# Optimization experiments

Hardware: AMD Instinct MI355X
Metric: run time of the kernel (lower is better)

Reference implementation:

```python
import jax, jax.numpy as jnp
import numpy as np

L, B, D, H = 2048, 2, 1024, 16
HD = D // H
DFF = 4 * D
EPS = 1e-5


def layernorm(x, g, b):
    mu = jnp.mean(x, axis=-1, keepdims=True)
    var = jnp.mean((x - mu) ** 2, axis=-1, keepdims=True)
    return (x - mu) * jax.lax.rsqrt(var + EPS) * g + b


def setup_inputs() -> dict:
    key = jax.random.key(0)
    ks = jax.random.split(key, 12)
    s = 0.02
    return {
        "x": jax.random.normal(ks[0], (L, B, D), jnp.float32),
        "ln1_g": jnp.ones((D,), jnp.float32),
        "ln1_b": jnp.zeros((D,), jnp.float32),
        "w_attn": jax.random.normal(ks[1], (D, 3 * D), jnp.float32) * s,
        "b_attn": jnp.zeros((3 * D,), jnp.float32),
        "w_proj": jax.random.normal(ks[2], (D, D), jnp.float32) * s,
        "b_proj": jnp.zeros((D,), jnp.float32),
        "ln2_g": jnp.ones((D,), jnp.float32),
        "ln2_b": jnp.zeros((D,), jnp.float32),
        "w_fc": jax.random.normal(ks[3], (D, DFF), jnp.float32) * s,
        "b_fc": jnp.zeros((DFF,), jnp.float32),
        "w_out": jax.random.normal(ks[4], (DFF, D), jnp.float32) * s,
        "b_out": jnp.zeros((D,), jnp.float32),
    }


def reference(x, ln1_g, ln1_b, w_attn, b_attn, w_proj, b_proj,
              ln2_g, ln2_b, w_fc, b_fc, w_out, b_out):
    # x: [L, B, D]
    h = layernorm(x, ln1_g, ln1_b)
    qkv = h @ w_attn + b_attn                     # [L, B, 3D]
    qkv = jnp.transpose(qkv, (1, 0, 2))            # [B, L, 3D]
    q, k, v = jnp.split(qkv, 3, axis=-1)

    def split_heads(t):                            # [B, L, D] -> [B, H, L, hd]
        return jnp.transpose(t.reshape(B, L, H, HD), (0, 2, 1, 3))

    q, k, v = split_heads(q), split_heads(k), split_heads(v)
    # present: stack of (key, value), key in [B,H,L,hd] layout (post transpose-back)
    present = jnp.stack((k, v))                    # [2, B, H, L, hd]

    scores = jnp.einsum('bhqd,bhkd->bhqk', q, k) / jnp.sqrt(jnp.float32(HD))
    w = jax.nn.softmax(scores, axis=-1)
    a = jnp.einsum('bhqk,bhkd->bhqd', w, v)        # [B, H, L, hd]
    a = jnp.transpose(a, (0, 2, 1, 3)).reshape(B, L, D)
    a = a @ w_proj + b_proj                        # [B, L, D]
    a = jnp.transpose(a, (1, 0, 2))                # [L, B, D]

    x = x + a
    m = jax.nn.gelu(layernorm(x, ln2_g, ln2_b) @ w_fc + b_fc) @ w_out + b_out
    x = x + m
    return x, present
```

## Files before the change

### kernel.cpp

```cpp
#include <hip/hip_runtime.h>
#include <stdint.h>

#define L_SEQ 2048
#define BATCH 2
#define DIM   1024
#define NH    16
#define HDIM  64
#define DFF_  4096
#define ROWS  (L_SEQ*BATCH)

#define QSCALE 0.18033688011112042f

typedef __attribute__((ext_vector_type(8))) short  bf16x8;
typedef __attribute__((ext_vector_type(4))) float  floatx4;

__device__ __forceinline__ unsigned short f2bf(float f) {
    union { float f; uint32_t u; } x; x.f = f;
    uint32_t r = x.u + 0x7fffu + ((x.u >> 16) & 1u);
    return (unsigned short)(r >> 16);
}
__device__ __forceinline__ float bf2f(unsigned short b) {
    union { uint32_t u; float f; } x; x.u = ((uint32_t)b) << 16;
    return x.f;
}
__device__ __forceinline__ uint32_t fbits(float f) {
    union { float f; uint32_t u; } x; x.f = f; return x.u;
}

__device__ __forceinline__ void load_lds16(const unsigned short* g, unsigned short* l) {
    __builtin_amdgcn_global_load_lds(
        (const __attribute__((address_space(1))) unsigned int*)g,
        (__attribute__((address_space(3))) unsigned int*)l, 16, 0, 0);
}

__global__ __launch_bounds__(256)
void transpose_all(const float* __restrict__ s0, unsigned short* __restrict__ d0,
                   const float* __restrict__ s1, unsigned short* __restrict__ d1,
                   const float* __restrict__ s2, unsigned short* __restrict__ d2,
                   const float* __restrict__ s3, unsigned short* __restrict__ d3)
{
    const int id = blockIdx.x;
    const float* src; unsigned short* dst; int K, N, local;
    if (id < 3072)      { src = s0; dst = d0; K = 1024; N = 3072; local = id; }
    else if (id < 4096) { src = s1; dst = d1; K = 1024; N = 1024; local = id - 3072; }
    else if (id < 8192) { src = s2; dst = d2; K = 1024; N = 4096; local = id - 4096; }
    else                { src = s3; dst = d3; K = 4096; N = 1024; local = id - 8192; }
    const int nN = N >> 5;
    const int bk = (local / nN) * 32, bn = (local % nN) * 32;

    __shared__ float tile[32][36];
    const int t = threadIdx.x;
    const int r = t >> 3, c4 = (t & 7) * 4;
    *(float4*)&tile[r][c4] = *(const float4*)(src + (size_t)(bk + r) * N + bn + c4);
    __syncthreads();
    ushort4 o;
    o.x = f2bf(tile[c4 + 0][r]);
    o.y = f2bf(tile[c4 + 1][r]);
    o.z = f2bf(tile[c4 + 2][r]);
    o.w = f2bf(tile[c4 + 3][r]);
    *(ushort4*)(dst + (size_t)(bn + r) * K + bk + c4) = o;
}

template<int INBF16>
__global__ __launch_bounds__(256)
void ln_rows(const void* __restrict__ xin, const float* __restrict__ g,
             const float* __restrict__ bta, unsigned short* __restrict__ out)
{
    const int row = blockIdx.x;
    const int t = threadIdx.x;
    float4 v;
    if (INBF16) {
        const ushort4 u = ((const ushort4*)((const unsigned short*)xin + (size_t)row * DIM))[t];
        v.x = bf2f(u.x); v.y = bf2f(u.y); v.z = bf2f(u.z); v.w = bf2f(u.w);
    } else {
        v = ((const float4*)((const float*)xin + (size_t)row * DIM))[t];
    }
    float s  = v.x + v.y + v.z + v.w;
    float s2 = v.x*v.x + v.y*v.y + v.z*v.z + v.w*v.w;
#pragma unroll
    for (int d = 1; d < 64; d <<= 1) { s += __shfl_xor(s, d, 64); s2 += __shfl_xor(s2, d, 64); }
    __shared__ float ss[4], ss2[4];
    const int w = t >> 6, lane = t & 63;
    if (lane == 0) { ss[w] = s; ss2[w] = s2; }
    __syncthreads();
    s  = ss[0] + ss[1] + ss[2] + ss[3];
    s2 = ss2[0] + ss2[1] + ss2[2] + ss2[3];
    const float mu   = s * (1.0f / DIM);
    const float var  = s2 * (1.0f / DIM) - mu * mu;
    const float rstd = rsqrtf(var + 1e-5f);
    const float4 gv = ((const float4*)g)[t];
    const float4 bv = ((const float4*)bta)[t];
    ushort4 o;
    o.x = f2bf((v.x - mu) * rstd * gv.x + bv.x);
    o.y = f2bf((v.y - mu) * rstd * gv.y + bv.y);
    o.z = f2bf((v.z - mu) * rstd * gv.z + bv.z);
    o.w = f2bf((v.w - mu) * rstd * gv.w + bv.w);
    *(ushort4*)(out + (size_t)row * DIM + t * 4) = o;
}

template<int GELU, int RESID, int OUTBF16, int MI, int SPLITK>
__global__ __launch_bounds__(256)
void gemm_bt(const unsigned short* __restrict__ A,
             const unsigned short* __restrict__ Bt,
             const float* __restrict__ bias,
             const void* __restrict__ resid,
             void* __restrict__ outp,
             float* __restrict__ part,
             int M, int N, int K)
{
    __shared__ unsigned short As[MI * 32 * 32];
    __shared__ unsigned short Bs[128 * 32];
    const int t = threadIdx.x;
    const int w = t >> 6, lane = t & 63;
    const int quad = lane >> 4, l16 = lane & 15;
    const int wm = (w >> 1) * (MI * 16), wn = (w & 1) * 64;
    const int bm = blockIdx.x * (MI * 32), bn = blockIdx.y * 128;

    const int srow = lane >> 2;
    const int scol = (lane & 3) * 8;

    const unsigned short* Ab = A  + (size_t)bm * K;
    const unsigned short* Bb = Bt + (size_t)bn * K;

    floatx4 acc[MI][4] = {};

    const int kspan = (SPLITK > 1) ? (K / SPLITK) : K;
    const int k0    = (SPLITK > 1) ? blockIdx.z * kspan : 0;

    for (int kc = k0; kc < k0 + kspan; kc += 32) {
        __syncthreads();
#pragma unroll
        for (int i = 0; i < MI / 2; ++i) {
            const int r0 = (i * 4 + w) * 16;
            load_lds16(Ab + (size_t)(r0 + srow) * K + kc + scol, As + r0 * 32);
        }
#pragma unroll
        for (int i = 0; i < 2; ++i) {
            const int r0 = (i * 4 + w) * 16;
            load_lds16(Bb + (size_t)(r0 + srow) * K + kc + scol, Bs + r0 * 32);
        }
        __syncthreads();
        bf16x8 af[MI], bf[4];
#pragma unroll
        for (int i = 0; i < MI; ++i) af[i] = *(const bf16x8*)(As + (wm + i*16 + l16) * 32 + quad * 8);
#pragma unroll
        for (int j = 0; j < 4; ++j) bf[j] = *(const bf16x8*)(Bs + (wn + j*16 + l16) * 32 + quad * 8);
#pragma unroll
        for (int i = 0; i < MI; ++i)
#pragma unroll
            for (int j = 0; j < 4; ++j)
                acc[i][j] = __builtin_amdgcn_mfma_f32_16x16x32_bf16(af[i], bf[j], acc[i][j], 0, 0, 0);
    }

    if (SPLITK > 1 && blockIdx.z > 0) {
        float* po = part + (size_t)(blockIdx.z - 1) * ((size_t)M * N);
#pragma unroll
        for (int i = 0; i < MI; ++i)
#pragma unroll
            for (int j = 0; j < 4; ++j) {
                const int col = bn + wn + j*16 + l16;
#pragma unroll
                for (int r = 0; r < 4; ++r) {
                    const int row = bm + wm + i*16 + quad*4 + r;
                    po[(size_t)row * N + col] = acc[i][j][r];
                }
            }
        return;
    }

#pragma unroll
    for (int i = 0; i < MI; ++i) {
#pragma unroll
        for (int j = 0; j < 4; ++j) {
            const int col = bn + wn + j*16 + l16;
            const float bv = bias[col];
#pragma unroll
            for (int r = 0; r < 4; ++r) {
                const int row = bm + wm + i*16 + quad*4 + r;
                float v = acc[i][j][r] + bv;
                if (RESID == 1) v += ((const float*)resid)[(size_t)row * N + col];
                if (RESID == 2) v += bf2f(((const unsigned short*)resid)[(size_t)row * N + col]);
                if (GELU) {
                    const float u = v;
                    float c = 2.302204225929898f * (u + 0.044715f * u * u * u);
                    c = fminf(c, 80.f);
                    const float e = exp2f(c);
                    v = u * (e / (1.0f + e));
                }
                if (OUTBF16) ((unsigned short*)outp)[(size_t)row * N + col] = f2bf(v);
                else         ((float*)outp)[(size_t)row * N + col] = v;
            }
        }
    }
}

#define SWZ32(p) ((p) ^ ((((p) >> 7) & 3) << 4))

template<int GELU, int RESID, int OUTBF16, int SPLITK>
__global__ __launch_bounds__(512, 2)
void gemm256b(const unsigned short* __restrict__ A,
              const unsigned short* __restrict__ Bt,
              const float* __restrict__ bias,
              const void* __restrict__ resid,
              void* __restrict__ outp,
              float* __restrict__ part,
              int M, int N, int K, int nbx)
{
    __shared__ unsigned short lds[32768];
    const int t = threadIdx.x;
    const int w = t >> 6, lane = t & 63;
    const int quad = lane >> 4, l16 = lane & 15;
    const int wr = w >> 2, wc = w & 3;

    const int nwg = gridDim.x;
    const int cpx = nwg >> 3;
    const int bid = (blockIdx.x & 7) * cpx + (blockIdx.x >> 3);
    const int bm = (bid % nbx) * 256, bn = (bid / nbx) * 256;

    const unsigned short* Ab = A  + (size_t)bm * K;
    const unsigned short* Bb = Bt + (size_t)bn * K;

    const int sh   = SWZ32(t * 16);
    const int rp0  = sh >> 6;
    const int colE = (sh & 63) >> 1;
    const int w0 = rp0 & 63, hb = rp0 >> 6;
    const size_t bOff0 = (size_t)rp0 * K + colE;
    const size_t bOff1 = (size_t)(128 + rp0) * K + colE;
    const size_t aOff0 = (size_t)(w0 + hb * 128)      * K + colE;
    const size_t aOff1 = (size_t)(w0 + hb * 128 + 64) * K + colE;

#define STGH(dstE_, srcp_, kta_, off_) \
    load_lds16((srcp_) + (size_t)(kta_) * 32 + (off_), lds + (dstE_) + w * 512)
#define BARF    do { __builtin_amdgcn_s_barrier(); asm volatile("" ::: "memory"); } while (0)
#define CL_PRE  do { asm volatile("s_waitcnt lgkmcnt(0)" ::: "memory");    \
                     __builtin_amdgcn_sched_barrier(0);                    \
                     __builtin_amdgcn_s_setprio(1); } while (0)
#define CL_POST do { __builtin_amdgcn_s_setprio(0);                        \
                     __builtin_amdgcn_sched_barrier(0); } while (0)

    floatx4 acc[8][4] = {};
    const int nt  = ((SPLITK > 1) ? (K / SPLITK) : K) >> 5;
    const int ktb = (SPLITK > 1) ? blockIdx.y * nt : 0;

    STGH(0,     Ab, ktb,     aOff0);  STGH(4096,  Ab, ktb,     aOff1);
    STGH(8192,  Bb, ktb,     bOff0);  STGH(12288, Bb, ktb,     bOff1);
    STGH(16384, Ab, ktb + 1, aOff0);  STGH(20480, Ab, ktb + 1, aOff1);
    STGH(24576, Bb, ktb + 1, bOff0);  STGH(28672, Bb, ktb + 1, bOff1);
    asm volatile("s_waitcnt vmcnt(4)" ::: "memory");
    BARF;

    for (int i = 0; i < nt; ++i) {
        const int cb = i & 1;
        const int i1 = (i + 1 < nt) ? i + 1 : nt - 1;
        const int i2 = (i + 2 < nt) ? i + 2 : nt - 1;
        const int oA = cb * 16384, oB = oA + 8192;
        const int xA = (cb ^ 1) * 16384;
        const char* Abase = (const char*)lds + cb * 32768;
        const char* Bbase = Abase + 16384;
        bf16x8 af[4], bf[4];

        STGH(xA + 4096, Ab, ktb + i1, aOff1);
#pragma unroll
        for (int mi = 0; mi < 4; ++mi) {
            const int p = (wr * 64 + mi * 16 + l16) * 64 + quad * 16;
            af[mi] = *(const bf16x8*)(Abase + SWZ32(p));
        }
#pragma unroll
        for (int nj = 0; nj < 4; ++nj) {
            const int p = (wc * 64 + nj * 16 + l16) * 64 + quad * 16;
            bf[nj] = *(const bf16x8*)(Bbase + SWZ32(p));
        }
        BARF;
        CL_PRE;
#pragma unroll
        for (int mi = 0; mi < 4; ++mi)
#pragma unroll
            for (int nj = 0; nj < 4; ++nj)
                acc[mi][nj] = __builtin_amdgcn_mfma_f32_16x16x32_bf16(af[mi], bf[nj], acc[mi][nj], 0, 0, 0);
        CL_POST;
        BARF;

        STGH(oB,        Bb, ktb + i2, bOff0);
        STGH(oB + 4096, Bb, ktb + i2, bOff1);
        STGH(oA,        Ab, ktb + i2, aOff0);
#pragma unroll
        for (int mi = 0; mi < 4; ++mi) {
            const int p = (128 + wr * 64 + mi * 16 + l16) * 64 + quad * 16;
            af[mi] = *(const bf16x8*)(Abase + SWZ32(p));
        }
        BARF;
        CL_PRE;
#pragma unroll
        for (int mi = 0; mi < 4; ++mi)
#pragma unroll
            for (int nj = 0; nj < 4; ++nj)
                acc[4 + mi][nj] = __builtin_amdgcn_mfma_f32_16x16x32_bf16(af[mi], bf[nj], acc[4 + mi][nj], 0, 0, 0);
        CL_POST;
        asm volatile("s_waitcnt vmcnt(3)" ::: "memory");
        BARF;
    }

    if (SPLITK > 1 && blockIdx.y > 0) {
        float* po = part + (size_t)(blockIdx.y - 1) * ((size_t)M * N);
#pragma unroll
        for (int mi = 0; mi < 8; ++mi)
#pragma unroll
            for (int nj = 0; nj < 4; ++nj) {
                const int col = bn + wc * 64 + nj * 16 + l16;
#pragma unroll
                for (int r = 0; r < 4; ++r) {
                    const int row = bm + wr * 128 + mi * 16 + quad * 4 + r;
                    po[(size_t)row * N + col] = acc[mi][nj][r];
                }
            }
        return;
    }

#pragma unroll
    for (int mi = 0; mi < 8; ++mi) {
#pragma unroll
        for (int nj = 0; nj < 4; ++nj) {
            const int col = bn + wc * 64 + nj * 16 + l16;
            const float bv = bias[col];
#pragma unroll
            for (int r = 0; r < 4; ++r) {
                const int row = bm + wr * 128 + mi * 16 + quad * 4 + r;
                float v = acc[mi][nj][r] + bv;
                if (RESID == 1) v += ((const float*)resid)[(size_t)row * N + col];
                if (RESID == 2) v += bf2f(((const unsigned short*)resid)[(size_t)row * N + col]);
                if (GELU) {
                    const float u = v;
                    float c = 2.302204225929898f * (u + 0.044715f * u * u * u);
                    c = fminf(c, 80.f);
                    const float e = exp2f(c);
                    v = u * (e / (1.0f + e));
                }
                if (OUTBF16) ((unsigned short*)outp)[(size_t)row * N + col] = f2bf(v);
                else         ((float*)outp)[(size_t)row * N + col] = v;
            }
        }
    }
#undef STGH
#undef BARF
#undef CL_PRE
#undef CL_POST
}

__global__ __launch_bounds__(256)
void splitk_add(const float* __restrict__ part, float* __restrict__ outp)
{
    const size_t i = ((size_t)blockIdx.x * 256 + threadIdx.x) * 4;
    float4 a = *(const float4*)(outp + i);
    const float4 p = *(const float4*)(part + i);
    a.x += p.x; a.y += p.y; a.z += p.z; a.w += p.w;
    *(float4*)(outp + i) = a;
}

__global__ __launch_bounds__(256)
void split_qkv(const unsigned short* __restrict__ qkv,
               unsigned short* __restrict__ q, unsigned short* __restrict__ k,
               float* __restrict__ present)
{
    const size_t idx = (size_t)blockIdx.x * 256 + threadIdx.x;
    const int g8  = idx & 7;
    const int l   = (idx >> 3) & 2047;
    const int bh  = (idx >> 14) & 31;
    const int sel = (int)(idx >> 19);
    const int b = bh >> 4, h = bh & 15;
    const unsigned short* src = qkv + (size_t)(l * BATCH + b) * (3 * DIM) + sel * DIM + h * HDIM + g8 * 8;
    const uint4 val = *(const uint4*)src;
    const unsigned short* sv = (const unsigned short*)&val;
    if (sel == 0) {
        unsigned short ov[8];
#pragma unroll
        for (int j = 0; j < 8; ++j) ov[j] = f2bf(bf2f(sv[j]) * QSCALE);
        *(uint4*)(q + ((size_t)bh * L_SEQ + l) * HDIM + g8 * 8) = *(uint4*)ov;
    } else {
        *(uint4*)(k + ((size_t)bh * L_SEQ + l) * HDIM + g8 * 8) = val;
        float* p = present + (((size_t)b * NH + h) * L_SEQ + l) * HDIM + (size_t)g8 * 8;
        float4 f0, f1;
        f0.x = bf2f(sv[0]); f0.y = bf2f(sv[1]); f0.z = bf2f(sv[2]); f0.w = bf2f(sv[3]);
        f1.x = bf2f(sv[4]); f1.y = bf2f(sv[5]); f1.z = bf2f(sv[6]); f1.w = bf2f(sv[7]);
        ((float4*)p)[0] = f0; ((float4*)p)[1] = f1;
    }
}

__global__ __launch_bounds__(256)
void transpose_v(const unsigned short* __restrict__ qkv, unsigned short* __restrict__ vt,
                 float* __restrict__ present)
{
    __shared__ unsigned short tile[64][72];
    const int lt = blockIdx.x;
    const int bh = blockIdx.y;
    const int b = bh >> 4, h = bh & 15;
    const int t = threadIdx.x;
#pragma unroll
    for (int i = 0; i < 2; ++i) {
        const int idx = i * 256 + t;
        const int l = idx >> 3, c = (idx & 7) * 8;
        const uint4 val =
            *(const uint4*)(qkv + (size_t)((lt * 64 + l) * BATCH + b) * (3 * DIM) + 2 * DIM + h * HDIM + c);
        *(uint4*)(&tile[l][c]) = val;
        const unsigned short* sv = (const unsigned short*)&val;
        float* p = present + ((((size_t)BATCH + b) * NH + h) * L_SEQ + lt * 64 + l) * HDIM + c;
        float4 f0, f1;
        f0.x = bf2f(sv[0]); f0.y = bf2f(sv[1]); f0.z = bf2f(sv[2]); f0.w = bf2f(sv[3]);
        f1.x = bf2f(sv[4]); f1.y = bf2f(sv[5]); f1.z = bf2f(sv[6]); f1.w = bf2f(sv[7]);
        ((float4*)p)[0] = f0; ((float4*)p)[1] = f1;
    }
    __syncthreads();
#pragma unroll
    for (int i = 0; i < 2; ++i) {
        const int idx = i * 256 + t;
        const int d = idx >> 3, l0 = (idx & 7) * 8;
        const int kk = l0 >> 3;
        ushort4 o[2];
        unsigned short* ov = (unsigned short*)o;
#pragma unroll
        for (int jj = 0; jj < 8; ++jj) {
            const int j = (jj + kk) & 7;
            ov[j] = tile[l0 + j][d];
        }
        *(uint4*)(vt + ((size_t)bh * HDIM + d) * L_SEQ + lt * 64 + l0) = *(uint4*)o;
    }
}

__global__ __launch_bounds__(256, 4)
void attn_kernel(const unsigned short* __restrict__ Q,
                 const unsigned short* __restrict__ Kk,
                 const unsigned short* __restrict__ Vt,
                 unsigned short* __restrict__ Opart,
                 float* __restrict__ Lpart)
{
    const int qt = blockIdx.x;
    const int ks = blockIdx.y;
    const int bh = blockIdx.z;
    const int b = bh >> 4, h = bh & 15;
    const int t = threadIdx.x, w = t >> 6, lane = t & 63;
    const int quad = lane >> 4, l16 = lane & 15;

    __shared__ unsigned short Ks[64][72];
    __shared__ unsigned short Vts[64][72];
    __shared__ unsigned short Ps[4][32][72];

    const size_t head_off = (size_t)bh * L_SEQ * HDIM;
    const int q_base = qt * 128 + w * 32;
    const int kt0 = ks * 1024;

    bf16x8 qf[2][2];
#pragma unroll
    for (int nf = 0; nf < 2; ++nf)
#pragma unroll
        for (int ds = 0; ds < 2; ++ds)
            qf[nf][ds] = *(const bf16x8*)(Q + head_off + (size_t)(q_base + nf*16 + l16) * HDIM + ds*32 + quad*8);

    const int sr = t >> 3;
    const int sc = (t & 7) * 8;

    floatx4 o[4][2] = {};
    float l_i[2] = {0.f, 0.f};

    for (int kt = kt0; kt < kt0 + 1024; kt += 64) {
        __syncthreads();
#pragma unroll
        for (int i = 0; i < 2; ++i) {
            const int row = sr + i * 32;
            *(uint4*)(&Ks[row][sc])  = *(const uint4*)(Kk + head_off + (size_t)(kt + row) * HDIM + sc);
            *(uint4*)(&Vts[row][sc]) = *(const uint4*)(Vt + head_off + (size_t)row * L_SEQ + kt + sc);
        }
        __syncthreads();

        floatx4 s[4][2] = {};
#pragma unroll
        for (int ds = 0; ds < 2; ++ds)
#pragma unroll
            for (int jt = 0; jt < 4; ++jt) {
                const bf16x8 kf = *(const bf16x8*)(&Ks[jt*16 + l16][ds*32 + quad*8]);
                s[jt][0] = __builtin_amdgcn_mfma_f32_16x16x32_bf16(kf, qf[0][ds], s[jt][0], 0, 0, 0);
                s[jt][1] = __builtin_amdgcn_mfma_f32_16x16x32_bf16(kf, qf[1][ds], s[jt][1], 0, 0, 0);
            }

#pragma unroll
        for (int nf = 0; nf < 2; ++nf)
#pragma unroll
            for (int jt = 0; jt < 4; ++jt) {
                const float p0 = exp2f(s[jt][nf][0]);
                const float p1 = exp2f(s[jt][nf][1]);
                const float p2 = exp2f(s[jt][nf][2]);
                const float p3 = exp2f(s[jt][nf][3]);
                l_i[nf] += (p0 + p1) + (p2 + p3);
                uint2 pk;
                pk.x = __builtin_amdgcn_perm(fbits(p1), fbits(p0), 0x07060302u);
                pk.y = __builtin_amdgcn_perm(fbits(p3), fbits(p2), 0x07060302u);
                *(uint2*)(&Ps[w][nf*16 + l16][jt*16 + quad*4]) = pk;
            }

#pragma unroll
        for (int kk = 0; kk < 2; ++kk) {
            const bf16x8 pf0 = *(const bf16x8*)(&Ps[w][l16]     [kk*32 + quad*8]);
            const bf16x8 pf1 = *(const bf16x8*)(&Ps[w][16 + l16][kk*32 + quad*8]);
#pragma unroll
            for (int dt = 0; dt < 4; ++dt) {
                const bf16x8 vf = *(const bf16x8*)(&Vts[dt*16 + l16][kk*32 + quad*8]);
                o[dt][0] = __builtin_amdgcn_mfma_f32_16x16x32_bf16(vf, pf0, o[dt][0], 0, 0, 0);
                o[dt][1] = __builtin_amdgcn_mfma_f32_16x16x32_bf16(vf, pf1, o[dt][1], 0, 0, 0);
            }
        }
    }

    unsigned short* Op = Opart + (size_t)ks * ROWS * DIM;
#pragma unroll
    for (int nf = 0; nf < 2; ++nf) {
        float l = l_i[nf];
        l += __shfl_xor(l, 16, 64);
        l += __shfl_xor(l, 32, 64);
        const int q = q_base + nf*16 + l16;
        if (quad == 0)
            Lpart[((size_t)ks * 32 + bh) * L_SEQ + q] = l;
#pragma unroll
        for (int dt = 0; dt < 4; ++dt) {
            ushort4 ov;
            ov.x = f2bf(o[dt][nf][0]); ov.y = f2bf(o[dt][nf][1]);
            ov.z = f2bf(o[dt][nf][2]); ov.w = f2bf(o[dt][nf][3]);
            *(ushort4*)(Op + (size_t)(q * BATCH + b) * DIM + h * HDIM + dt*16 + quad*4) = ov;
        }
    }
}

__global__ __launch_bounds__(256)
void attn_merge(const unsigned short* __restrict__ Opart,
                const float* __restrict__ Lpart,
                unsigned short* __restrict__ Aout)
{
    const int row = blockIdx.x;
    const int q = row >> 1, b = row & 1;
    const int t = threadIdx.x;
    const int col = t * 4;
    const int h = col >> 6;
    const int bh = b * 16 + h;
    const float l0 = Lpart[(size_t)bh * L_SEQ + q];
    const float l1 = Lpart[((size_t)32 + bh) * L_SEQ + q];
    const float inv = 1.0f / (l0 + l1);
    const ushort4 o0 = *(const ushort4*)(Opart + (size_t)row * DIM + col);
    const ushort4 o1 = *(const ushort4*)(Opart + (size_t)ROWS * DIM + (size_t)row * DIM + col);
    ushort4 ov;
    ov.x = f2bf((bf2f(o0.x) + bf2f(o1.x)) * inv);
    ov.y = f2bf((bf2f(o0.y) + bf2f(o1.y)) * inv);
    ov.z = f2bf((bf2f(o0.z) + bf2f(o1.z)) * inv);
    ov.w = f2bf((bf2f(o0.w) + bf2f(o1.w)) * inv);
    *(ushort4*)(Aout + (size_t)row * DIM + col) = ov;
}

extern "C" void kernel_launch(void* const* d_in, const int* in_sizes, int n_in,
                              void* d_out, int out_size, void* d_ws, size_t ws_size,
                              hipStream_t stream)
{
    const float* x      = (const float*)d_in[0];
    const float* ln1_g  = (const float*)d_in[1];
    const float* ln1_b  = (const float*)d_in[2];
    const float* w_attn = (const float*)d_in[3];
    const float* b_attn = (const float*)d_in[4];
    const float* w_proj = (const float*)d_in[5];
    const float* b_proj = (const float*)d_in[6];
    const float* ln2_g  = (const float*)d_in[7];
    const float* ln2_b  = (const float*)d_in[8];
    const float* w_fc   = (const float*)d_in[9];
    const float* b_fc   = (const float*)d_in[10];
    const float* w_out  = (const float*)d_in[11];
    const float* b_out  = (const float*)d_in[12];

    char* ws = (char*)d_ws;
    unsigned short* watT   = (unsigned short*)(ws + 0);
    unsigned short* wprojT = (unsigned short*)(ws + 6291456);
    unsigned short* wfcT   = (unsigned short*)(ws + 8388608);
    unsigned short* woutT  = (unsigned short*)(ws + 16777216);
    unsigned short* h      = (unsigned short*)(ws + 25165824);
    unsigned short* qkv    = (unsigned short*)(ws + 33554432);
    unsigned short* opart  = (unsigned short*)(ws + 33554432);
    float*          lpart  = (float*)(ws + 50331648);
    unsigned short* mws    = (unsigned short*)(ws + 33554432);
    unsigned short* qw     = (unsigned short*)(ws + 58720256);
    unsigned short* kw     = (unsigned short*)(ws + 67108864);
    unsigned short* vt     = (unsigned short*)(ws + 75497472);
    unsigned short* aw     = (unsigned short*)(ws + 83886080);
    unsigned short* x2     = (unsigned short*)(ws + 92274688);
    float*          kpart  = (float*)(ws + 75497472);

    float* xout    = (float*)d_out;
    float* present = (float*)d_out + 4194304;

    transpose_all<<<12288, 256, 0, stream>>>(w_attn, watT, w_proj, wprojT, w_fc, wfcT, w_out, woutT);

    ln_rows<0><<<ROWS, 256, 0, stream>>>(x, ln1_g, ln1_b, h);
    gemm256b<0,0,1,1><<<dim3(192), 512, 0, stream>>>(h, watT, b_attn, nullptr, qkv, nullptr, ROWS, 3*DIM, DIM, 16);
    split_qkv<<<4096, 256, 0, stream>>>(qkv, qw, kw, present);
    transpose_v<<<dim3(32, 32), 256, 0, stream>>>(qkv, vt, present);
    attn_kernel<<<dim3(16, 2, 32), 256, 0, stream>>>(qw, kw, vt, opart, lpart);
    attn_merge<<<ROWS, 256, 0, stream>>>(opart, lpart, aw);
    gemm_bt<0,1,1,2,1><<<dim3(64, 8), 256, 0, stream>>>(aw, wprojT, b_proj, x, x2, nullptr, ROWS, DIM, DIM);
    ln_rows<1><<<ROWS, 256, 0, stream>>>(x2, ln2_g, ln2_b, h);
    gemm256b<1,0,1,1><<<dim3(256), 512, 0, stream>>>(h, wfcT, b_fc, nullptr, mws, nullptr, ROWS, DFF_, DIM, 16);
    gemm_bt<0,2,0,4,2><<<dim3(32, 8, 2), 256, 0, stream>>>(mws, woutT, b_out, x2, xout, kpart, ROWS, DIM, DFF_);
    splitk_add<<<4096, 256, 0, stream>>>(kpart, xout);
}
```

Before: 403.0 us.

## Double-buffer attention K/V tiles with async global-to-LDS loads and XOR swizzle

The attention kernel now stages K and V tiles into two LDS buffers using direct global-to-LDS loads (load_lds16), prefetching two tiles ahead so memory latency overlaps the MFMA work. The padded LDS arrays are replaced by an XOR-swizzled layout to avoid bank conflicts without padding. K fragments are loaded into registers before the buffer is refilled. This adds barriers per iteration and register pressure, and relies on vmcnt accounting being correct.

```diff
diff --git a/kernel.cpp b/kernel.cpp
--- a/kernel.cpp
+++ b/kernel.cpp
@@ -425,6 +425,8 @@
     }
 }
 
+#define SWZA(p) ((p) ^ ((((p) >> 7) & 7) << 4))
+
 __global__ __launch_bounds__(256, 4)
 void attn_kernel(const unsigned short* __restrict__ Q,
                  const unsigned short* __restrict__ Kk,
@@ -439,8 +441,8 @@
     const int t = threadIdx.x, w = t >> 6, lane = t & 63;
     const int quad = lane >> 4, l16 = lane & 15;
 
-    __shared__ unsigned short Ks[64][72];
-    __shared__ unsigned short Vts[64][72];
+    __shared__ unsigned short Ksb[2][4096];
+    __shared__ unsigned short Vsb[2][4096];
     __shared__ unsigned short Ps[4][32][72];
 
     const size_t head_off = (size_t)bh * L_SEQ * HDIM;
@@ -454,30 +456,58 @@
         for (int ds = 0; ds < 2; ++ds)
             qf[nf][ds] = *(const bf16x8*)(Q + head_off + (size_t)(q_base + nf*16 + l16) * HDIM + ds*32 + quad*8);
 
-    const int sr = t >> 3;
-    const int sc = (t & 7) * 8;
+    const int pA = t * 16, pB = 4096 + t * 16;
+    const int cA = (pA & 127) ^ (((pA >> 7) & 7) << 4);
+    const int cB = (pB & 127) ^ (((pB >> 7) & 7) << 4);
+    const int rA = pA >> 7, rB = pB >> 7;
+    const size_t kOff0 = (size_t)rA * HDIM + (cA >> 1);
+    const size_t kOff1 = (size_t)rB * HDIM + (cB >> 1);
+    const size_t vOff0 = (size_t)rA * L_SEQ + (cA >> 1);
+    const size_t vOff1 = (size_t)rB * L_SEQ + (cB >> 1);
+
+#define STAGE_K(buf_, kt_) do {                                            \
+        const unsigned short* g_ = Kk + head_off + (size_t)(kt_) * HDIM;   \
+        load_lds16(g_ + kOff0, Ksb[buf_] + w * 512);                       \
+        load_lds16(g_ + kOff1, Ksb[buf_] + 2048 + w * 512);                \
+    } while (0)
+#define STAGE_V(buf_, kt_) do {                                            \
+        const unsigned short* g_ = Vt + head_off + (kt_);                  \
+        load_lds16(g_ + vOff0, Vsb[buf_] + w * 512);                       \
+        load_lds16(g_ + vOff1, Vsb[buf_] + 2048 + w * 512);                \
+    } while (0)
 
     floatx4 o[4][2] = {};
     float l_i[2] = {0.f, 0.f};
 
-    for (int kt = kt0; kt < kt0 + 1024; kt += 64) {
+    STAGE_K(0, kt0);      STAGE_V(0, kt0);
+    STAGE_K(1, kt0 + 64); STAGE_V(1, kt0 + 64);
+    asm volatile("s_waitcnt vmcnt(4)" ::: "memory");
+    __syncthreads();
+
+    for (int it = 0; it < 16; ++it) {
+        const int cb = it & 1;
+        const int i2 = (it + 2 < 16) ? it + 2 : 15;
+        const unsigned short* Kl = Ksb[cb];
+        const unsigned short* Vl = Vsb[cb];
+
+        bf16x8 kf[2][4];
+#pragma unroll
+        for (int ds = 0; ds < 2; ++ds)
+#pragma unroll
+            for (int jt = 0; jt < 4; ++jt) {
+                const int p = (jt*16 + l16) * 128 + ds*64 + quad*16;
+                kf[ds][jt] = *(const bf16x8*)((const char*)Kl + SWZA(p));
+            }
         __syncthreads();
-#pragma unroll
-        for (int i = 0; i < 2; ++i) {
-            const int row = sr + i * 32;
-            *(uint4*)(&Ks[row][sc])  = *(const uint4*)(Kk + head_off + (size_t)(kt + row) * HDIM + sc);
-            *(uint4*)(&Vts[row][sc]) = *(const uint4*)(Vt + head_off + (size_t)row * L_SEQ + kt + sc);
-        }
-        __syncthreads();
+        STAGE_K(cb, kt0 + i2 * 64);
 
         floatx4 s[4][2] = {};
 #pragma unroll
         for (int ds = 0; ds < 2; ++ds)
 #pragma unroll
             for (int jt = 0; jt < 4; ++jt) {
-                const bf16x8 kf = *(const bf16x8*)(&Ks[jt*16 + l16][ds*32 + quad*8]);
-                s[jt][0] = __builtin_amdgcn_mfma_f32_16x16x32_bf16(kf, qf[0][ds], s[jt][0], 0, 0, 0);
-                s[jt][1] = __builtin_amdgcn_mfma_f32_16x16x32_bf16(kf, qf[1][ds], s[jt][1], 0, 0, 0);
+                s[jt][0] = __builtin_amdgcn_mfma_f32_16x16x32_bf16(kf[ds][jt], qf[0][ds], s[jt][0], 0, 0, 0);
+                s[jt][1] = __builtin_amdgcn_mfma_f32_16x16x32_bf16(kf[ds][jt], qf[1][ds], s[jt][1], 0, 0, 0);
             }
 
 #pragma unroll
@@ -501,11 +531,16 @@
             const bf16x8 pf1 = *(const bf16x8*)(&Ps[w][16 + l16][kk*32 + quad*8]);
 #pragma unroll
             for (int dt = 0; dt < 4; ++dt) {
-                const bf16x8 vf = *(const bf16x8*)(&Vts[dt*16 + l16][kk*32 + quad*8]);
+                const int p = (dt*16 + l16) * 128 + kk*64 + quad*16;
+                const bf16x8 vf = *(const bf16x8*)((const char*)Vl + SWZA(p));
                 o[dt][0] = __builtin_amdgcn_mfma_f32_16x16x32_bf16(vf, pf0, o[dt][0], 0, 0, 0);
                 o[dt][1] = __builtin_amdgcn_mfma_f32_16x16x32_bf16(vf, pf1, o[dt][1], 0, 0, 0);
             }
         }
+        __syncthreads();
+        STAGE_V(cb, kt0 + i2 * 64);
+        asm volatile("s_waitcnt vmcnt(4)" ::: "memory");
+        __syncthreads();
     }
 
     unsigned short* Op = Opart + (size_t)ks * ROWS * DIM;
@@ -525,6 +560,8 @@
             *(ushort4*)(Op + (size_t)(q * BATCH + b) * DIM + h * HDIM + dt*16 + quad*4) = ov;
         }
     }
+#undef STAGE_K
+#undef STAGE_V
 }
 
 __global__ __launch_bounds__(256)
```

After: 413.4 us. 1.03x slower.

## Prefetch K/V tiles into registers and XOR-swizzle attention LDS tiles

Applied to the files above, without the earlier changes.

The attention kernel now loads the next 64-key K and V^T tile into registers while computing on the current tile, then writes it to LDS after the compute. This hides global-load latency behind the MFMA work. The padded LDS arrays are replaced by unpadded 128-byte rows with an XOR swizzle for K, V^T and P, to avoid bank conflicts without the padding. The gemm256b template also loses its unused split-K and residual parameters, which is cleanup only. The prefetch adds registers and an extra barrier per iteration, which may lower occupancy.

```diff
diff --git a/kernel.cpp b/kernel.cpp
--- a/kernel.cpp
+++ b/kernel.cpp
@@ -196,14 +196,12 @@
 
 #define SWZ32(p) ((p) ^ ((((p) >> 7) & 3) << 4))
 
-template<int GELU, int RESID, int OUTBF16, int SPLITK>
+template<int GELU, int OUTBF16>
 __global__ __launch_bounds__(512, 2)
 void gemm256b(const unsigned short* __restrict__ A,
               const unsigned short* __restrict__ Bt,
               const float* __restrict__ bias,
-              const void* __restrict__ resid,
               void* __restrict__ outp,
-              float* __restrict__ part,
               int M, int N, int K, int nbx)
 {
     __shared__ unsigned short lds[32768];
@@ -239,13 +237,12 @@
                      __builtin_amdgcn_sched_barrier(0); } while (0)
 
     floatx4 acc[8][4] = {};
-    const int nt  = ((SPLITK > 1) ? (K / SPLITK) : K) >> 5;
-    const int ktb = (SPLITK > 1) ? blockIdx.y * nt : 0;
-
-    STGH(0,     Ab, ktb,     aOff0);  STGH(4096,  Ab, ktb,     aOff1);
-    STGH(8192,  Bb, ktb,     bOff0);  STGH(12288, Bb, ktb,     bOff1);
-    STGH(16384, Ab, ktb + 1, aOff0);  STGH(20480, Ab, ktb + 1, aOff1);
-    STGH(24576, Bb, ktb + 1, bOff0);  STGH(28672, Bb, ktb + 1, bOff1);
+    const int nt = K >> 5;
+
+    STGH(0,     Ab, 0, aOff0);  STGH(4096,  Ab, 0, aOff1);
+    STGH(8192,  Bb, 0, bOff0);  STGH(12288, Bb, 0, bOff1);
+    STGH(16384, Ab, 1, aOff0);  STGH(20480, Ab, 1, aOff1);
+    STGH(24576, Bb, 1, bOff0);  STGH(28672, Bb, 1, bOff1);
     asm volatile("s_waitcnt vmcnt(4)" ::: "memory");
     BARF;
 
@@ -259,7 +256,7 @@
         const char* Bbase = Abase + 16384;
         bf16x8 af[4], bf[4];
 
-        STGH(xA + 4096, Ab, ktb + i1, aOff1);
+        STGH(xA + 4096, Ab, i1, aOff1);
 #pragma unroll
         for (int mi = 0; mi < 4; ++mi) {
             const int p = (wr * 64 + mi * 16 + l16) * 64 + quad * 16;
@@ -280,9 +277,9 @@
         CL_POST;
         BARF;
 
-        STGH(oB,        Bb, ktb + i2, bOff0);
-        STGH(oB + 4096, Bb, ktb + i2, bOff1);
-        STGH(oA,        Ab, ktb + i2, aOff0);
+        STGH(oB,        Bb, i2, bOff0);
+        STGH(oB + 4096, Bb, i2, bOff1);
+        STGH(oA,        Ab, i2, aOff0);
 #pragma unroll
         for (int mi = 0; mi < 4; ++mi) {
             const int p = (128 + wr * 64 + mi * 16 + l16) * 64 + quad * 16;
@@ -300,22 +297,6 @@
         BARF;
     }
 
-    if (SPLITK > 1 && blockIdx.y > 0) {
-        float* po = part + (size_t)(blockIdx.y - 1) * ((size_t)M * N);
-#pragma unroll
-        for (int mi = 0; mi < 8; ++mi)
-#pragma unroll
-            for (int nj = 0; nj < 4; ++nj) {
-                const int col = bn + wc * 64 + nj * 16 + l16;
-#pragma unroll
-                for (int r = 0; r < 4; ++r) {
-                    const int row = bm + wr * 128 + mi * 16 + quad * 4 + r;
-                    po[(size_t)row * N + col] = acc[mi][nj][r];
-                }
-            }
-        return;
-    }
-
 #pragma unroll
     for (int mi = 0; mi < 8; ++mi) {
 #pragma unroll
@@ -326,8 +307,6 @@
             for (int r = 0; r < 4; ++r) {
                 const int row = bm + wr * 128 + mi * 16 + quad * 4 + r;
                 float v = acc[mi][nj][r] + bv;
-                if (RESID == 1) v += ((const float*)resid)[(size_t)row * N + col];
-                if (RESID == 2) v += bf2f(((const unsigned short*)resid)[(size_t)row * N + col]);
                 if (GELU) {
                     const float u = v;
                     float c = 2.302204225929898f * (u + 0.044715f * u * u * u);
@@ -425,6 +404,8 @@
     }
 }
 
+#define SWZA(p) ((p) ^ ((((p) >> 7) & 7) << 4))
+
 __global__ __launch_bounds__(256, 4)
 void attn_kernel(const unsigned short* __restrict__ Q,
                  const unsigned short* __restrict__ Kk,
@@ -439,9 +420,9 @@
     const int t = threadIdx.x, w = t >> 6, lane = t & 63;
     const int quad = lane >> 4, l16 = lane & 15;
 
-    __shared__ unsigned short Ks[64][72];
-    __shared__ unsigned short Vts[64][72];
-    __shared__ unsigned short Ps[4][32][72];
+    __shared__ unsigned short Ks[4096];
+    __shared__ unsigned short Vts[4096];
+    __shared__ unsigned short Ps[4][2048];
 
     const size_t head_off = (size_t)bh * L_SEQ * HDIM;
     const int q_base = qt * 128 + w * 32;
@@ -455,27 +436,43 @@
             qf[nf][ds] = *(const bf16x8*)(Q + head_off + (size_t)(q_base + nf*16 + l16) * HDIM + ds*32 + quad*8);
 
     const int sr = t >> 3;
-    const int sc = (t & 7) * 8;
+    const int c8 = t & 7;
+    const int sc = c8 * 8;
+    const int wb = sr * 128 + ((c8 * 16) ^ ((sr & 7) << 4));
+    const int wb2 = wb + 32 * 128;
+
+    uint4 kreg0, kreg1, vreg0, vreg1;
+
+#define LOAD_TILE(kt_) do {                                                              \
+        kreg0 = *(const uint4*)(Kk + head_off + (size_t)((kt_) + sr) * HDIM + sc);       \
+        kreg1 = *(const uint4*)(Kk + head_off + (size_t)((kt_) + sr + 32) * HDIM + sc);  \
+        vreg0 = *(const uint4*)(Vt + head_off + (size_t)sr * L_SEQ + (kt_) + sc);        \
+        vreg1 = *(const uint4*)(Vt + head_off + (size_t)(sr + 32) * L_SEQ + (kt_) + sc); \
+    } while (0)
+#define WRITE_TILE() do {                                                                \
+        *(uint4*)((char*)Ks + wb)   = kreg0;                                             \
+        *(uint4*)((char*)Ks + wb2)  = kreg1;                                             \
+        *(uint4*)((char*)Vts + wb)  = vreg0;                                             \
+        *(uint4*)((char*)Vts + wb2) = vreg1;                                             \
+    } while (0)
 
     floatx4 o[4][2] = {};
     float l_i[2] = {0.f, 0.f};
 
-    for (int kt = kt0; kt < kt0 + 1024; kt += 64) {
-        __syncthreads();
-#pragma unroll
-        for (int i = 0; i < 2; ++i) {
-            const int row = sr + i * 32;
-            *(uint4*)(&Ks[row][sc])  = *(const uint4*)(Kk + head_off + (size_t)(kt + row) * HDIM + sc);
-            *(uint4*)(&Vts[row][sc]) = *(const uint4*)(Vt + head_off + (size_t)row * L_SEQ + kt + sc);
-        }
-        __syncthreads();
+    LOAD_TILE(kt0);
+    WRITE_TILE();
+    __syncthreads();
+
+    for (int it = 0; it < 16; ++it) {
+        if (it + 1 < 16) LOAD_TILE(kt0 + (it + 1) * 64);
 
         floatx4 s[4][2] = {};
 #pragma unroll
         for (int ds = 0; ds < 2; ++ds)
 #pragma unroll
             for (int jt = 0; jt < 4; ++jt) {
-                const bf16x8 kf = *(const bf16x8*)(&Ks[jt*16 + l16][ds*32 + quad*8]);
+                const int p = (jt*16 + l16) * 128 + ds*64 + quad*16;
+                const bf16x8 kf = *(const bf16x8*)((const char*)Ks + SWZA(p));
                 s[jt][0] = __builtin_amdgcn_mfma_f32_16x16x32_bf16(kf, qf[0][ds], s[jt][0], 0, 0, 0);
                 s[jt][1] = __builtin_amdgcn_mfma_f32_16x16x32_bf16(kf, qf[1][ds], s[jt][1], 0, 0, 0);
             }
@@ -492,20 +489,28 @@
                 uint2 pk;
                 pk.x = __builtin_amdgcn_perm(fbits(p1), fbits(p0), 0x07060302u);
                 pk.y = __builtin_amdgcn_perm(fbits(p3), fbits(p2), 0x07060302u);
-                *(uint2*)(&Ps[w][nf*16 + l16][jt*16 + quad*4]) = pk;
+                const int q = nf*16 + l16;
+                const int kb = jt*32 + quad*8;
+                *(uint2*)((char*)Ps[w] + q*128 + (kb ^ ((q & 7) << 4))) = pk;
             }
 
 #pragma unroll
         for (int kk = 0; kk < 2; ++kk) {
-            const bf16x8 pf0 = *(const bf16x8*)(&Ps[w][l16]     [kk*32 + quad*8]);
-            const bf16x8 pf1 = *(const bf16x8*)(&Ps[w][16 + l16][kk*32 + quad*8]);
+            const int cbyte = kk*64 + quad*16;
+            const bf16x8 pf0 = *(const bf16x8*)((const char*)Ps[w] + l16*128      + (cbyte ^ ((l16 & 7) << 4)));
+            const bf16x8 pf1 = *(const bf16x8*)((const char*)Ps[w] + (16+l16)*128 + (cbyte ^ ((l16 & 7) << 4)));
 #pragma unroll
             for (int dt = 0; dt < 4; ++dt) {
-                const bf16x8 vf = *(const bf16x8*)(&Vts[dt*16 + l16][kk*32 + quad*8]);
+                const int p = (dt*16 + l16) * 128 + cbyte;
+                const bf16x8 vf = *(const bf16x8*)((const char*)Vts + SWZA(p));
                 o[dt][0] = __builtin_amdgcn_mfma_f32_16x16x32_bf16(vf, pf0, o[dt][0], 0, 0, 0);
                 o[dt][1] = __builtin_amdgcn_mfma_f32_16x16x32_bf16(vf, pf1, o[dt][1], 0, 0, 0);
             }
         }
+
+        __syncthreads();
+        if (it + 1 < 16) WRITE_TILE();
+        __syncthreads();
     }
 
     unsigned short* Op = Opart + (size_t)ks * ROWS * DIM;
@@ -525,6 +530,8 @@
             *(ushort4*)(Op + (size_t)(q * BATCH + b) * DIM + h * HDIM + dt*16 + quad*4) = ov;
         }
     }
+#undef LOAD_TILE
+#undef WRITE_TILE
 }
 
 __global__ __launch_bounds__(256)
@@ -592,14 +599,14 @@
     transpose_all<<<12288, 256, 0, stream>>>(w_attn, watT, w_proj, wprojT, w_fc, wfcT, w_out, woutT);
 
     ln_rows<0><<<ROWS, 256, 0, stream>>>(x, ln1_g, ln1_b, h);
-    gemm256b<0,0,1,1><<<dim3(192), 512, 0, stream>>>(h, watT, b_attn, nullptr, qkv, nullptr, ROWS, 3*DIM, DIM, 16);
+    gemm256b<0,1><<<dim3(192), 512, 0, stream>>>(h, watT, b_attn, qkv, ROWS, 3*DIM, DIM, 16);
     split_qkv<<<4096, 256, 0, stream>>>(qkv, qw, kw, present);
     transpose_v<<<dim3(32, 32), 256, 0, stream>>>(qkv, vt, present);
     attn_kernel<<<dim3(16, 2, 32), 256, 0, stream>>>(qw, kw, vt, opart, lpart);
     attn_merge<<<ROWS, 256, 0, stream>>>(opart, lpart, aw);
     gemm_bt<0,1,1,2,1><<<dim3(64, 8), 256, 0, stream>>>(aw, wprojT, b_proj, x, x2, nullptr, ROWS, DIM, DIM);
     ln_rows<1><<<ROWS, 256, 0, stream>>>(x2, ln2_g, ln2_b, h);
-    gemm256b<1,0,1,1><<<dim3(256), 512, 0, stream>>>(h, wfcT, b_fc, nullptr, mws, nullptr, ROWS, DFF_, DIM, 16);
+    gemm256b<1,1><<<dim3(256), 512, 0, stream>>>(h, wfcT, b_fc, mws, ROWS, DFF_, DIM, 16);
     gemm_bt<0,2,0,4,2><<<dim3(32, 8, 2), 256, 0, stream>>>(mws, woutT, b_out, x2, xout, kpart, ROWS, DIM, DFF_);
     splitk_add<<<4096, 256, 0, stream>>>(kpart, xout);
 }
```

After: 403.7 us. Within noise of the previous version (+0.2%).
